# Kernel tuning notes

Measured on AMD Instinct MI355X. Metric: run time of the kernel, lower is better.

## Reference

```python
import jax, jax.numpy as jnp
import numpy as np

Q_DIM, KV_DIM, H = 64, 64, 4


def setup_inputs() -> dict:
    key = jax.random.key(0)
    ks = jax.random.split(key, 8)
    b, t = 8, 128
    q_x = jax.random.normal(ks[0], (b, t, Q_DIM), dtype=jnp.float32)
    kv_x = jax.random.normal(ks[1], (b, t, t - 1, KV_DIM), dtype=jnp.float32)
    # nn.Linear weights: (out_features, in_features), applied as x @ W.T
    Wk = jax.random.normal(ks[2], (KV_DIM * H, KV_DIM), dtype=jnp.float32) * 0.05
    Wq = jax.random.normal(ks[3], (KV_DIM * H, Q_DIM), dtype=jnp.float32) * 0.05
    Wv = jax.random.normal(ks[4], (KV_DIM * H, KV_DIM), dtype=jnp.float32) * 0.05
    bias = jax.random.uniform(ks[5], (KV_DIM,), minval=-0.1, maxval=0.1, dtype=jnp.float32)
    Ws = jax.random.normal(ks[6], (1, KV_DIM), dtype=jnp.float32) * 0.05
    bs = jax.random.normal(ks[7], (1,), dtype=jnp.float32) * 0.05
    return {"q_x": q_x, "kv_x": kv_x, "Wk": Wk, "Wq": Wq, "Wv": Wv,
            "bias": bias, "Ws": Ws, "bs": bs}


def reference(q_x, kv_x, Wk, Wq, Wv, bias, Ws, bs):
    b, t, tm1, k = kv_x.shape  # tm1 == t-1
    h = H
    # keys: (b, t, t-1, h, k)
    keys = (kv_x @ Wk.T).reshape(b, t, tm1, h, k)
    # queries: (b, t, 1, h, k)
    queries = (q_x @ Wq.T).reshape(b, t, 1, h, k)
    # additive tanh score projected to scalar per (b,t,n,h)
    act = jnp.tanh(keys + queries + bias)
    score = jnp.einsum('btnhk,k->btnh', act, Ws[0]) + bs[0]
    # softmax over the t-1 key axis (dim=2)
    w = jax.nn.softmax(score, axis=2)  # (b, t, t-1, h)
    values = (kv_x @ Wv.T).reshape(b, t, tm1, h, k)
    # weighted sum over t-1
    x = jnp.einsum('btnh,btnhk->bthk', w, values)
    return x.reshape(b, t, h * k)
```

## Files before the change

### kernel.cpp

```cpp
#include <hip/hip_runtime.h>
#include <math.h>

#define B 8
#define T 128
#define NKEY 127
#define NPAD 128
#define KDIM 64
#define NH 4
#define CH 256

typedef short short8 __attribute__((ext_vector_type(8)));
typedef float floatx4 __attribute__((ext_vector_type(4)));

__device__ __forceinline__ float fast_tanh(float x) {
    float e = __expf(2.f * x);
    float r = __builtin_amdgcn_rcpf(e + 1.f);
    return fmaf(-2.f, r, 1.f);
}

__device__ __forceinline__ void split8(const float4& a, const float4& b,
                                       short8& hi, short8& lo) {
    float x[8] = {a.x, a.y, a.z, a.w, b.x, b.y, b.z, b.w};
    #pragma unroll
    for (int i = 0; i < 8; ++i) {
        unsigned u = __float_as_uint(x[i]);
        hi[i] = (short)(u >> 16);
        float l = x[i] - __uint_as_float(u & 0xFFFF0000u);
        lo[i] = (short)(__float_as_uint(l) >> 16);
    }
}

__device__ __forceinline__ void rne8(const float4& a, const float4& b, short8& hi) {
    float x[8] = {a.x, a.y, a.z, a.w, b.x, b.y, b.z, b.w};
    #pragma unroll
    for (int i = 0; i < 8; ++i) {
        unsigned u = __float_as_uint(x[i]);
        u += 0x7FFFu + ((u >> 16) & 1u);
        hi[i] = (short)(u >> 16);
    }
}

__global__ __launch_bounds__(256, 2)
void attn_kernel(const float* __restrict__ q_x,
                 const float* __restrict__ kv_x,
                 const float* __restrict__ Wk,
                 const float* __restrict__ Wq,
                 const float* __restrict__ Wv,
                 const float* __restrict__ bias,
                 const float* __restrict__ Ws,
                 const float* __restrict__ bs,
                 float* __restrict__ out)
{
    __shared__ __align__(16) short bh_lds[16][64][8];
    __shared__ __align__(16) short bl_lds[16][64][8];
    __shared__ float qb_lds[CH];
    __shared__ float p_lds[NH][NPAD];
    __shared__ __align__(16) float wkv_lds[NH][KDIM];

    const int bt   = blockIdx.x;
    const int tid  = threadIdx.x;
    const int h    = tid >> 6;
    const int lane = tid & 63;
    const int col  = lane & 15;
    const int quad = lane >> 4;

    const float* __restrict__ kvg = kv_x + (size_t)bt * NKEY * KDIM;

    #pragma unroll
    for (int w = 0; w < 4; ++w) {
        const int chunk = w * 4 + h;
        const int nt = chunk >> 1, ks = chunk & 1;
        const int n  = nt * 16 + (lane & 15);
        const int k0 = ks * 32 + (lane >> 4) * 8;
        float4 a = make_float4(0.f, 0.f, 0.f, 0.f);
        float4 b = make_float4(0.f, 0.f, 0.f, 0.f);
        if (n < NKEY) {
            const float* p = kvg + (size_t)n * KDIM + k0;
            a = *(const float4*)p;
            b = *(const float4*)(p + 4);
        }
        short8 hi, lo;
        split8(a, b, hi, lo);
        *(short8*)&bh_lds[chunk][lane][0] = hi;
        *(short8*)&bl_lds[chunk][lane][0] = lo;
    }

    {
        const float4* Wq4 = (const float4*)(Wq + (size_t)tid * KDIM);
        const float4* q4g = (const float4*)(q_x + (size_t)bt * KDIM);
        float4 qa = {0.f, 0.f, 0.f, 0.f};
        #pragma unroll
        for (int i = 0; i < 16; ++i) {
            float4 w = Wq4[i];
            float4 q4 = q4g[i];
            qa.x = fmaf(q4.x, w.x, qa.x);
            qa.y = fmaf(q4.y, w.y, qa.y);
            qa.z = fmaf(q4.z, w.z, qa.z);
            qa.w = fmaf(q4.w, w.w, qa.w);
        }
        qb_lds[tid] = (qa.x + qa.y) + (qa.z + qa.w) + bias[tid & 63];
    }

    short8 ahi[4][2];
    #pragma unroll
    for (int jt = 0; jt < 4; ++jt)
        #pragma unroll
        for (int ks = 0; ks < 2; ++ks) {
            const float* wrow = Wk + (size_t)(h * 64 + jt * 16 + col) * KDIM
                                   + ks * 32 + quad * 8;
            float4 a = *(const float4*)wrow;
            float4 b = *(const float4*)(wrow + 4);
            rne8(a, b, ahi[jt][ks]);
        }

    __syncthreads();

    float qbv[4][4], wsv[4][4];
    #pragma unroll
    for (int jt = 0; jt < 4; ++jt)
        #pragma unroll
        for (int r = 0; r < 4; ++r) {
            int j = jt * 16 + quad * 4 + r;
            qbv[jt][r] = qb_lds[h * 64 + j];
            wsv[jt][r] = Ws[j];
        }

    #pragma unroll
    for (int nt = 0; nt < 8; ++nt) {
        short8 bhi0 = *(const short8*)&bh_lds[nt * 2 + 0][lane][0];
        short8 blo0 = *(const short8*)&bl_lds[nt * 2 + 0][lane][0];
        short8 bhi1 = *(const short8*)&bh_lds[nt * 2 + 1][lane][0];
        short8 blo1 = *(const short8*)&bl_lds[nt * 2 + 1][lane][0];

        floatx4 acc[4];
        #pragma unroll
        for (int jt = 0; jt < 4; ++jt) {
            floatx4 c = {0.f, 0.f, 0.f, 0.f};
            c = __builtin_amdgcn_mfma_f32_16x16x32_bf16(ahi[jt][0], bhi0, c, 0, 0, 0);
            c = __builtin_amdgcn_mfma_f32_16x16x32_bf16(ahi[jt][1], bhi1, c, 0, 0, 0);
            c = __builtin_amdgcn_mfma_f32_16x16x32_bf16(ahi[jt][0], blo0, c, 0, 0, 0);
            c = __builtin_amdgcn_mfma_f32_16x16x32_bf16(ahi[jt][1], blo1, c, 0, 0, 0);
            acc[jt] = c;
        }

        float partial = 0.f;
        #pragma unroll
        for (int jt = 0; jt < 4; ++jt)
            #pragma unroll
            for (int r = 0; r < 4; ++r)
                partial = fmaf(fast_tanh(acc[jt][r] + qbv[jt][r]), wsv[jt][r], partial);
        partial += __shfl_xor(partial, 16, 64);
        partial += __shfl_xor(partial, 32, 64);
        if (lane < 16) p_lds[h][nt * 16 + lane] = partial;
    }

    float invl;
    {
        float s_a = p_lds[h][lane];
        float s_b = p_lds[h][64 + lane];
        if (lane == 63) s_b = -1e30f;
        float mx = fmaxf(s_a, s_b);
        #pragma unroll
        for (int off = 32; off > 0; off >>= 1)
            mx = fmaxf(mx, __shfl_xor(mx, off, 64));
        float pa = __expf(s_a - mx);
        float pb = __expf(s_b - mx);
        float ls = pa + pb;
        #pragma unroll
        for (int off = 32; off > 0; off >>= 1)
            ls += __shfl_xor(ls, off, 64);
        invl = 1.f / ls;
        p_lds[h][lane]      = pa;
        p_lds[h][64 + lane] = pb;
    }

    {
        const float* kvl = kvg + lane;
        float w0 = 0.f, w1 = 0.f, w2 = 0.f, w3 = 0.f;
        #pragma unroll 8
        for (int n4 = 0; n4 < NPAD; n4 += 4) {
            float4 p4 = *(const float4*)&p_lds[h][n4];
            const int n3 = (n4 + 3 < NKEY) ? (n4 + 3) : 0;
            w0 = fmaf(p4.x, kvl[(size_t)(n4 + 0) * KDIM], w0);
            w1 = fmaf(p4.y, kvl[(size_t)(n4 + 1) * KDIM], w1);
            w2 = fmaf(p4.z, kvl[(size_t)(n4 + 2) * KDIM], w2);
            w3 = fmaf(p4.w, kvl[(size_t)n3 * KDIM], w3);
        }
        wkv_lds[h][lane] = ((w0 + w1) + (w2 + w3)) * invl;
    }

    {
        const float4* Wv4 = (const float4*)(Wv + (size_t)tid * KDIM);
        const float4* wv_row = (const float4*)wkv_lds[h];
        float4 oa = {0.f, 0.f, 0.f, 0.f};
        #pragma unroll
        for (int i = 0; i < 16; ++i) {
            float4 w = Wv4[i];
            float4 c = wv_row[i];
            oa.x = fmaf(c.x, w.x, oa.x);
            oa.y = fmaf(c.y, w.y, oa.y);
            oa.z = fmaf(c.z, w.z, oa.z);
            oa.w = fmaf(c.w, w.w, oa.w);
        }
        out[(size_t)bt * CH + tid] = (oa.x + oa.y) + (oa.z + oa.w);
    }
}

extern "C" void kernel_launch(void* const* d_in, const int* in_sizes, int n_in,
                              void* d_out, int out_size, void* d_ws, size_t ws_size,
                              hipStream_t stream) {
    const float* q_x  = (const float*)d_in[0];
    const float* kv_x = (const float*)d_in[1];
    const float* Wk   = (const float*)d_in[2];
    const float* Wq   = (const float*)d_in[3];
    const float* Wv   = (const float*)d_in[4];
    const float* bias = (const float*)d_in[5];
    const float* Ws   = (const float*)d_in[6];
    const float* bs   = (const float*)d_in[7];
    float* out = (float*)d_out;

    attn_kernel<<<dim3(B * T), dim3(256), 0, stream>>>(
        q_x, kv_x, Wk, Wq, Wv, bias, Ws, bs, out);
}
```

Baseline: 116.5 us.

## Split heads across two blocks per row and switch split-bf16 MFMA to fp16

The grid doubles so each block handles two heads, and within a block two waves split each head's 64 output channels, with partial scores combined through LDS. The hi/lo bf16 split with four MFMAs per tile becomes a single fp16 MFMA pair, with the query+bias term fed in as the accumulator init. LDS use shrinks and launch bounds rise to allow more resident blocks. The costs are that kv_x rows are loaded and converted twice (once per head-pair block), extra barriers are added, and fp16 rounding of the inputs reduces accuracy.

```diff
diff --git a/kernel.cpp b/kernel.cpp
--- a/kernel.cpp
+++ b/kernel.cpp
@@ -4,12 +4,11 @@
 #define B 8
 #define T 128
 #define NKEY 127
-#define NPAD 128
 #define KDIM 64
 #define NH 4
 #define CH 256
 
-typedef short short8 __attribute__((ext_vector_type(8)));
+typedef _Float16 half8 __attribute__((ext_vector_type(8)));
 typedef float floatx4 __attribute__((ext_vector_type(4)));
 
 __device__ __forceinline__ float fast_tanh(float x) {
@@ -18,29 +17,16 @@
     return fmaf(-2.f, r, 1.f);
 }
 
-__device__ __forceinline__ void split8(const float4& a, const float4& b,
-                                       short8& hi, short8& lo) {
-    float x[8] = {a.x, a.y, a.z, a.w, b.x, b.y, b.z, b.w};
-    #pragma unroll
-    for (int i = 0; i < 8; ++i) {
-        unsigned u = __float_as_uint(x[i]);
-        hi[i] = (short)(u >> 16);
-        float l = x[i] - __uint_as_float(u & 0xFFFF0000u);
-        lo[i] = (short)(__float_as_uint(l) >> 16);
-    }
-}
-
-__device__ __forceinline__ void rne8(const float4& a, const float4& b, short8& hi) {
-    float x[8] = {a.x, a.y, a.z, a.w, b.x, b.y, b.z, b.w};
-    #pragma unroll
-    for (int i = 0; i < 8; ++i) {
-        unsigned u = __float_as_uint(x[i]);
-        u += 0x7FFFu + ((u >> 16) & 1u);
-        hi[i] = (short)(u >> 16);
-    }
-}
-
-__global__ __launch_bounds__(256, 2)
+__device__ __forceinline__ half8 cvt8(const float4& a, const float4& b) {
+    half8 h;
+    h[0] = (_Float16)a.x; h[1] = (_Float16)a.y;
+    h[2] = (_Float16)a.z; h[3] = (_Float16)a.w;
+    h[4] = (_Float16)b.x; h[5] = (_Float16)b.y;
+    h[6] = (_Float16)b.z; h[7] = (_Float16)b.w;
+    return h;
+}
+
+__global__ __launch_bounds__(256, 4)
 void attn_kernel(const float* __restrict__ q_x,
                  const float* __restrict__ kv_x,
                  const float* __restrict__ Wk,
@@ -51,27 +37,32 @@
                  const float* __restrict__ bs,
                  float* __restrict__ out)
 {
-    __shared__ __align__(16) short bh_lds[16][64][8];
-    __shared__ __align__(16) short bl_lds[16][64][8];
-    __shared__ float qb_lds[CH];
-    __shared__ float p_lds[NH][NPAD];
-    __shared__ __align__(16) float wkv_lds[NH][KDIM];
-
-    const int bt   = blockIdx.x;
+    __shared__ __align__(16) _Float16 bh_lds[16][64][8];
+    __shared__ __align__(16) float qb_lds[128];
+    __shared__ __align__(16) float pp_lds[4][128];
+
+    float* const probs = (float*)bh_lds;
+    float* const wkv2  = (float*)bh_lds + 256;
+
+    const int bt   = blockIdx.x & 1023;
+    const int hp   = blockIdx.x >> 10;
     const int tid  = threadIdx.x;
-    const int h    = tid >> 6;
+    const int wid  = tid >> 6;
     const int lane = tid & 63;
     const int col  = lane & 15;
     const int quad = lane >> 4;
+    const int h2   = wid & 1;
+    const int role = wid >> 1;
+    const int hg   = hp * 2 + h2;
 
     const float* __restrict__ kvg = kv_x + (size_t)bt * NKEY * KDIM;
 
     #pragma unroll
     for (int w = 0; w < 4; ++w) {
-        const int chunk = w * 4 + h;
+        const int chunk = w * 4 + wid;
         const int nt = chunk >> 1, ks = chunk & 1;
-        const int n  = nt * 16 + (lane & 15);
-        const int k0 = ks * 32 + (lane >> 4) * 8;
+        const int n  = nt * 16 + col;
+        const int k0 = ks * 32 + quad * 8;
         float4 a = make_float4(0.f, 0.f, 0.f, 0.f);
         float4 b = make_float4(0.f, 0.f, 0.f, 0.f);
         if (n < NKEY) {
@@ -79,18 +70,28 @@
             a = *(const float4*)p;
             b = *(const float4*)(p + 4);
         }
-        short8 hi, lo;
-        split8(a, b, hi, lo);
-        *(short8*)&bh_lds[chunk][lane][0] = hi;
-        *(short8*)&bl_lds[chunk][lane][0] = lo;
-    }
-
-    {
-        const float4* Wq4 = (const float4*)(Wq + (size_t)tid * KDIM);
-        const float4* q4g = (const float4*)(q_x + (size_t)bt * KDIM);
-        float4 qa = {0.f, 0.f, 0.f, 0.f};
-        #pragma unroll
-        for (int i = 0; i < 16; ++i) {
+        *(half8*)&bh_lds[chunk][lane][0] = cvt8(a, b);
+    }
+
+    half8 ah[2][2];
+    #pragma unroll
+    for (int jtl = 0; jtl < 2; ++jtl)
+        #pragma unroll
+        for (int ks = 0; ks < 2; ++ks) {
+            const float* wrow = Wk + (size_t)(hg * 64 + role * 32 + jtl * 16 + col) * KDIM
+                                   + ks * 32 + quad * 8;
+            float4 a = *(const float4*)wrow;
+            float4 b = *(const float4*)(wrow + 4);
+            ah[jtl][ks] = cvt8(a, b);
+        }
+
+    {
+        const int c = tid >> 1, kh = tid & 1;
+        const float4* Wq4 = (const float4*)(Wq + (size_t)(hp * 128 + c) * KDIM + kh * 32);
+        const float4* q4g = (const float4*)(q_x + (size_t)bt * KDIM + kh * 32);
+        float4 qa = make_float4(0.f, 0.f, 0.f, 0.f);
+        #pragma unroll
+        for (int i = 0; i < 8; ++i) {
             float4 w = Wq4[i];
             float4 q4 = q4g[i];
             qa.x = fmaf(q4.x, w.x, qa.x);
@@ -98,66 +99,46 @@
             qa.z = fmaf(q4.z, w.z, qa.z);
             qa.w = fmaf(q4.w, w.w, qa.w);
         }
-        qb_lds[tid] = (qa.x + qa.y) + (qa.z + qa.w) + bias[tid & 63];
-    }
-
-    short8 ahi[4][2];
-    #pragma unroll
-    for (int jt = 0; jt < 4; ++jt)
-        #pragma unroll
-        for (int ks = 0; ks < 2; ++ks) {
-            const float* wrow = Wk + (size_t)(h * 64 + jt * 16 + col) * KDIM
-                                   + ks * 32 + quad * 8;
-            float4 a = *(const float4*)wrow;
-            float4 b = *(const float4*)(wrow + 4);
-            rne8(a, b, ahi[jt][ks]);
-        }
-
-    __syncthreads();
-
-    float qbv[4][4], wsv[4][4];
-    #pragma unroll
-    for (int jt = 0; jt < 4; ++jt)
-        #pragma unroll
-        for (int r = 0; r < 4; ++r) {
-            int j = jt * 16 + quad * 4 + r;
-            qbv[jt][r] = qb_lds[h * 64 + j];
-            wsv[jt][r] = Ws[j];
-        }
+        float r = (qa.x + qa.y) + (qa.z + qa.w);
+        r += __shfl_xor(r, 1, 64);
+        if (kh == 0) qb_lds[c] = r + bias[c & 63];
+    }
+
+    __syncthreads();
+
+    floatx4 qb4[2];
+    float4  wsv[2];
+    #pragma unroll
+    for (int jtl = 0; jtl < 2; ++jtl) {
+        qb4[jtl] = *(const floatx4*)&qb_lds[h2 * 64 + role * 32 + jtl * 16 + quad * 4];
+        wsv[jtl] = *(const float4*)&Ws[role * 32 + jtl * 16 + quad * 4];
+    }
 
     #pragma unroll
     for (int nt = 0; nt < 8; ++nt) {
-        short8 bhi0 = *(const short8*)&bh_lds[nt * 2 + 0][lane][0];
-        short8 blo0 = *(const short8*)&bl_lds[nt * 2 + 0][lane][0];
-        short8 bhi1 = *(const short8*)&bh_lds[nt * 2 + 1][lane][0];
-        short8 blo1 = *(const short8*)&bl_lds[nt * 2 + 1][lane][0];
-
-        floatx4 acc[4];
-        #pragma unroll
-        for (int jt = 0; jt < 4; ++jt) {
-            floatx4 c = {0.f, 0.f, 0.f, 0.f};
-            c = __builtin_amdgcn_mfma_f32_16x16x32_bf16(ahi[jt][0], bhi0, c, 0, 0, 0);
-            c = __builtin_amdgcn_mfma_f32_16x16x32_bf16(ahi[jt][1], bhi1, c, 0, 0, 0);
-            c = __builtin_amdgcn_mfma_f32_16x16x32_bf16(ahi[jt][0], blo0, c, 0, 0, 0);
-            c = __builtin_amdgcn_mfma_f32_16x16x32_bf16(ahi[jt][1], blo1, c, 0, 0, 0);
-            acc[jt] = c;
-        }
-
+        half8 b0 = *(const half8*)&bh_lds[nt * 2 + 0][lane][0];
+        half8 b1 = *(const half8*)&bh_lds[nt * 2 + 1][lane][0];
         float partial = 0.f;
         #pragma unroll
-        for (int jt = 0; jt < 4; ++jt)
+        for (int jtl = 0; jtl < 2; ++jtl) {
+            floatx4 c = qb4[jtl];
+            c = __builtin_amdgcn_mfma_f32_16x16x32_f16(ah[jtl][0], b0, c, 0, 0, 0);
+            c = __builtin_amdgcn_mfma_f32_16x16x32_f16(ah[jtl][1], b1, c, 0, 0, 0);
             #pragma unroll
             for (int r = 0; r < 4; ++r)
-                partial = fmaf(fast_tanh(acc[jt][r] + qbv[jt][r]), wsv[jt][r], partial);
+                partial = fmaf(fast_tanh(c[r]), wsv[jtl][r], partial);
+        }
         partial += __shfl_xor(partial, 16, 64);
         partial += __shfl_xor(partial, 32, 64);
-        if (lane < 16) p_lds[h][nt * 16 + lane] = partial;
-    }
+        if (lane < 16) pp_lds[wid][nt * 16 + lane] = partial;
+    }
+
+    __syncthreads();
 
     float invl;
     {
-        float s_a = p_lds[h][lane];
-        float s_b = p_lds[h][64 + lane];
+        float s_a = pp_lds[h2][lane]      + pp_lds[2 + h2][lane];
+        float s_b = pp_lds[h2][64 + lane] + pp_lds[2 + h2][64 + lane];
         if (lane == 63) s_b = -1e30f;
         float mx = fmaxf(s_a, s_b);
         #pragma unroll
@@ -170,39 +151,53 @@
         for (int off = 32; off > 0; off >>= 1)
             ls += __shfl_xor(ls, off, 64);
         invl = 1.f / ls;
-        p_lds[h][lane]      = pa;
-        p_lds[h][64 + lane] = pb;
-    }
+        if (role == 0) {
+            probs[h2 * 128 + lane]      = pa;
+            probs[h2 * 128 + 64 + lane] = pb;
+        }
+    }
+
+    __syncthreads();
 
     {
         const float* kvl = kvg + lane;
+        const float* pr  = probs + h2 * 128;
+        const int n0 = role * 64;
         float w0 = 0.f, w1 = 0.f, w2 = 0.f, w3 = 0.f;
-        #pragma unroll 8
-        for (int n4 = 0; n4 < NPAD; n4 += 4) {
-            float4 p4 = *(const float4*)&p_lds[h][n4];
+        #pragma unroll 4
+        for (int n4 = n0; n4 < n0 + 64; n4 += 4) {
+            float4 p4 = *(const float4*)&pr[n4];
             const int n3 = (n4 + 3 < NKEY) ? (n4 + 3) : 0;
             w0 = fmaf(p4.x, kvl[(size_t)(n4 + 0) * KDIM], w0);
             w1 = fmaf(p4.y, kvl[(size_t)(n4 + 1) * KDIM], w1);
             w2 = fmaf(p4.z, kvl[(size_t)(n4 + 2) * KDIM], w2);
             w3 = fmaf(p4.w, kvl[(size_t)n3 * KDIM], w3);
         }
-        wkv_lds[h][lane] = ((w0 + w1) + (w2 + w3)) * invl;
-    }
-
-    {
-        const float4* Wv4 = (const float4*)(Wv + (size_t)tid * KDIM);
-        const float4* wv_row = (const float4*)wkv_lds[h];
-        float4 oa = {0.f, 0.f, 0.f, 0.f};
-        #pragma unroll
-        for (int i = 0; i < 16; ++i) {
+        wkv2[wid * 64 + lane] = ((w0 + w1) + (w2 + w3)) * invl;
+    }
+
+    __syncthreads();
+
+    {
+        const int c = tid >> 1, kh = tid & 1;
+        const int hc = c >> 6;
+        const float4* wa  = (const float4*)&wkv2[hc * 64 + kh * 32];
+        const float4* wb  = (const float4*)&wkv2[(2 + hc) * 64 + kh * 32];
+        const float4* Wv4 = (const float4*)(Wv + (size_t)(hp * 128 + c) * KDIM + kh * 32);
+        float4 oa = make_float4(0.f, 0.f, 0.f, 0.f);
+        #pragma unroll
+        for (int i = 0; i < 8; ++i) {
             float4 w = Wv4[i];
-            float4 c = wv_row[i];
-            oa.x = fmaf(c.x, w.x, oa.x);
-            oa.y = fmaf(c.y, w.y, oa.y);
-            oa.z = fmaf(c.z, w.z, oa.z);
-            oa.w = fmaf(c.w, w.w, oa.w);
-        }
-        out[(size_t)bt * CH + tid] = (oa.x + oa.y) + (oa.z + oa.w);
+            float4 v = wa[i];
+            float4 u = wb[i];
+            oa.x = fmaf(v.x + u.x, w.x, oa.x);
+            oa.y = fmaf(v.y + u.y, w.y, oa.y);
+            oa.z = fmaf(v.z + u.z, w.z, oa.z);
+            oa.w = fmaf(v.w + u.w, w.w, oa.w);
+        }
+        float r = (oa.x + oa.y) + (oa.z + oa.w);
+        r += __shfl_xor(r, 1, 64);
+        if (kh == 0) out[(size_t)bt * CH + hp * 128 + c] = r;
     }
 }
 
@@ -219,6 +214,6 @@
     const float* bs   = (const float*)d_in[7];
     float* out = (float*)d_out;
 
-    attn_kernel<<<dim3(B * T), dim3(256), 0, stream>>>(
+    attn_kernel<<<dim3(2 * B * T), dim3(256), 0, stream>>>(
         q_x, kv_x, Wk, Wq, Wv, bias, Ws, bs, out);
 }
```

Result: slower. 123.6 us (+6.1%).
